# Kernel optimization log

Hardware: AMD Instinct MI355X
Metric: run time of the kernel (lower is better)

Reference implementation:

```python
import jax, jax.numpy as jnp
import numpy as np

X_DIM, H_DIM, SEQ, BATCH = 38, 128, 128, 2048


def _gru_step(h, x_t, Wih, Whh, bih, bhh):
    # PyTorch GRUCell: gates ordered (r, z, n)
    gi = x_t @ Wih.T + bih          # [B, 3H]
    gh = h @ Whh.T + bhh            # [B, 3H]
    gi_r, gi_z, gi_n = jnp.split(gi, 3, axis=-1)
    gh_r, gh_z, gh_n = jnp.split(gh, 3, axis=-1)
    r = jax.nn.sigmoid(gi_r + gh_r)
    z = jax.nn.sigmoid(gi_z + gh_z)
    n = jnp.tanh(gi_n + r * gh_n)
    return (1.0 - z) * n + z * h


def setup_inputs() -> dict:
    key = jax.random.key(0)
    ks = jax.random.split(key, 12)
    s_x = 1.0 / np.sqrt(H_DIM)
    inp = {
        "x": jax.random.normal(ks[0], (BATCH, SEQ, X_DIM), dtype=jnp.float32),
        "enc_Wih": jax.random.uniform(ks[1], (3 * H_DIM, X_DIM), minval=-s_x, maxval=s_x, dtype=jnp.float32),
        "enc_Whh": jax.random.uniform(ks[2], (3 * H_DIM, H_DIM), minval=-s_x, maxval=s_x, dtype=jnp.float32),
        "enc_bih": jax.random.uniform(ks[3], (3 * H_DIM,), minval=-s_x, maxval=s_x, dtype=jnp.float32),
        "enc_bhh": jax.random.uniform(ks[4], (3 * H_DIM,), minval=-s_x, maxval=s_x, dtype=jnp.float32),
        "dec_Wih": jax.random.uniform(ks[5], (3 * H_DIM, X_DIM), minval=-s_x, maxval=s_x, dtype=jnp.float32),
        "dec_Whh": jax.random.uniform(ks[6], (3 * H_DIM, H_DIM), minval=-s_x, maxval=s_x, dtype=jnp.float32),
        "dec_bih": jax.random.uniform(ks[7], (3 * H_DIM,), minval=-s_x, maxval=s_x, dtype=jnp.float32),
        "dec_bhh": jax.random.uniform(ks[8], (3 * H_DIM,), minval=-s_x, maxval=s_x, dtype=jnp.float32),
        "lin_W": jax.random.uniform(ks[9], (X_DIM, H_DIM), minval=-s_x, maxval=s_x, dtype=jnp.float32),
        "lin_b": jax.random.uniform(ks[10], (X_DIM,), minval=-s_x, maxval=s_x, dtype=jnp.float32),
    }
    return inp


def reference(x, enc_Wih, enc_Whh, enc_bih, enc_bhh,
              dec_Wih, dec_Whh, dec_bih, dec_bhh, lin_W, lin_b):
    B, T, _ = x.shape
    H = enc_Whh.shape[1]
    X = x.shape[-1]
    xs = jnp.swapaxes(x, 0, 1)  # [T, B, X]

    # Encoder: scan GRUCell over time, h0 = zeros
    def enc_step(h, x_t):
        h = _gru_step(h, x_t, enc_Wih, enc_Whh, enc_bih, enc_bhh)
        return h, None
    h0 = jnp.zeros((B, H), dtype=x.dtype)
    h_enc, _ = jax.lax.scan(enc_step, h0, xs)

    def dec_step(carry, _):
        h, o_prev = carry
        h = _gru_step(h, o_prev, dec_Wih, dec_Whh, dec_bih, dec_bhh)
        o = h @ lin_W.T + lin_b  # [B, X]
        return (h, o), o
    go = jnp.zeros((B, X), dtype=x.dtype)
    _, outs = jax.lax.scan(dec_step, (h_enc, go), None, length=T)  # [T, B, X]
    return jnp.swapaxes(outs, 0, 1)  # [B, T, X]
```

## Files before the change

### kernel.cpp

```cpp
#include <hip/hip_runtime.h>
#include <cstdint>


#define T_SEQ 128
#define X_DIM 38
#define H_DIM 128
#define B_TOT 2048
#define BT    8
#define HS    136
#define XK    40
#define XCH   64

#define HB_BYTES   (2 * BT * HS * 2)
#define XC_BYTES   ((XCH + 1) * BT * XK * 2)
#define SMEM_BYTES (HB_BYTES + XC_BYTES)

typedef _Float16 half8 __attribute__((ext_vector_type(8)));
typedef float    f32x4 __attribute__((ext_vector_type(4)));

#define MF(a, b, c) __builtin_amdgcn_mfma_f32_16x16x32_f16((a), (b), (c), 0, 0, 0)

__device__ __forceinline__ float fast_sigmoid(float x) {
    return __builtin_amdgcn_rcpf(1.0f + __expf(-x));
}
__device__ __forceinline__ float fast_tanh(float x) {
    return 1.0f - 2.0f * __builtin_amdgcn_rcpf(1.0f + __expf(2.0f * x));
}

#define XG_CALC(TLOC, OUTr, OUTz, OUTn)                                        \
    do {                                                                       \
        const _Float16* xr_ = xchunk + ((TLOC) * BT + arow) * XK;              \
        half8 x0_ = *(const half8*)(xr_ + quad * 8);                           \
        half8 x1_ = *(const half8*)(xr_ + 32);                                 \
        OUTr = MF(x0_, wxe[0][0], vb_r);                                       \
        OUTr = MF(x1_, wxe[0][1], OUTr);                                       \
        OUTz = MF(x0_, wxe[1][0], vb_z);                                       \
        OUTz = MF(x1_, wxe[1][1], OUTz);                                       \
        OUTn = MF(x0_, wxe[2][0], vb_ngi);                                     \
        OUTn = MF(x1_, wxe[2][1], OUTn);                                       \
    } while (0)

#define ENC_STEP(HRD, HWR, TLOC, INr, INz, INn, OUTr, OUTz, OUTn)              \
    do {                                                                       \
        const _Float16* xn_ = xchunk + (((TLOC) + 1) * BT + arow) * XK;        \
        half8 xn0_ = *(const half8*)(xn_ + quad * 8);                          \
        half8 xn1_ = *(const half8*)(xn_ + 32);                                \
        const _Float16* hb_ = (HRD) + arow * HS + quad * 8;                    \
        half8 h0_ = *(const half8*)(hb_ + 0 * 32);                             \
        half8 h1_ = *(const half8*)(hb_ + 1 * 32);                             \
        half8 h2_ = *(const half8*)(hb_ + 2 * 32);                             \
        half8 h3_ = *(const half8*)(hb_ + 3 * 32);                             \
        f32x4 ar_ = MF(h0_, wh[0][0], INr);                                    \
        ar_ = MF(h1_, wh[0][1], ar_);                                          \
        f32x4 arB_ = MF(h2_, wh[0][2], vzero);                                 \
        arB_ = MF(h3_, wh[0][3], arB_);                                        \
        f32x4 az_ = MF(h0_, wh[1][0], INz);                                    \
        az_ = MF(h1_, wh[1][1], az_);                                          \
        f32x4 azB_ = MF(h2_, wh[1][2], vzero);                                 \
        azB_ = MF(h3_, wh[1][3], azB_);                                        \
        f32x4 gn_ = MF(h0_, wh[2][0], vb_ngh);                                 \
        gn_ = MF(h1_, wh[2][1], gn_);                                          \
        f32x4 gnB_ = MF(h2_, wh[2][2], vzero);                                 \
        gnB_ = MF(h3_, wh[2][3], gnB_);                                        \
        _Pragma("unroll")                                                      \
        for (int e_ = 0; e_ < 2; ++e_) {                                       \
            const int rg_ = 2 * e_;           \
            const float r_ = fast_sigmoid(ar_[rg_] + arB_[rg_]);               \
            const float z_ = fast_sigmoid(az_[rg_] + azB_[rg_]);               \
            const float n_ = fast_tanh(INn[rg_] + r_ * (gn_[rg_] + gnB_[rg_]));\
            const float h_ = n_ + z_ * (hold[e_] - n_);                        \
            hold[e_] = h_;                                                     \
            (HWR)[(2 * quad + e_) * HS + j] = (_Float16)h_;                    \
        }                                                                      \
        OUTr = MF(xn0_, wxe[0][0], vb_r);           \
        OUTr = MF(xn1_, wxe[0][1], OUTr);           \
        OUTz = MF(xn0_, wxe[1][0], vb_z);                                      \
        OUTz = MF(xn1_, wxe[1][1], OUTz);                                      \
        OUTn = MF(xn0_, wxe[2][0], vb_ngi);                                    \
        OUTn = MF(xn1_, wxe[2][1], OUTn);                                      \
        __syncthreads();                                                       \
    } while (0)

#define DEC_STEP(HRD, HWR, TOUT)                                               \
    do {                                                                       \
        const _Float16* hb_ = (HRD) + arow * HS + quad * 8;                    \
        half8 h0_ = *(const half8*)(hb_ + 0 * 32);                             \
        half8 h1_ = *(const half8*)(hb_ + 1 * 32);                             \
        half8 h2_ = *(const half8*)(hb_ + 2 * 32);                             \
        half8 h3_ = *(const half8*)(hb_ + 3 * 32);                             \
        if (wv < 3) {             \
            f32x4 al_ = MF(h0_, wl[0], vb_lb);                                 \
            al_ = MF(h1_, wl[1], al_);                                         \
            f32x4 alB_ = MF(h2_, wl[2], vzero);                                \
            alB_ = MF(h3_, wl[3], alB_);                                       \
            if (nv) {                                                          \
                out[obase0 + (size_t)(TOUT) * X_DIM] = al_[0] + alB_[0];       \
                out[obase1 + (size_t)(TOUT) * X_DIM] = al_[2] + alB_[2];       \
            }                                                                  \
        }                                                                      \
        f32x4 ar_ = MF(h0_, wh[0][0], vd_r);                                   \
        ar_ = MF(h1_, wh[0][1], ar_);                                          \
        f32x4 arB_ = MF(h2_, wh[0][2], vzero);                                 \
        arB_ = MF(h3_, wh[0][3], arB_);                                        \
        f32x4 az_ = MF(h0_, wh[1][0], vd_z);                                   \
        az_ = MF(h1_, wh[1][1], az_);                                          \
        f32x4 azB_ = MF(h2_, wh[1][2], vzero);                                 \
        azB_ = MF(h3_, wh[1][3], azB_);                                        \
        f32x4 gn_ = MF(h0_, wh[2][0], vd_gh);                                  \
        gn_ = MF(h1_, wh[2][1], gn_);                                          \
        f32x4 gnB_ = MF(h2_, wh[2][2], vzero);                                 \
        gnB_ = MF(h3_, wh[2][3], gnB_);                                        \
        f32x4 gi_ = MF(h0_, wxn[0], vd_gi);                                    \
        gi_ = MF(h1_, wxn[1], gi_);                                            \
        f32x4 giB_ = MF(h2_, wxn[2], vzero);                                   \
        giB_ = MF(h3_, wxn[3], giB_);                                          \
        _Pragma("unroll")                                                      \
        for (int e_ = 0; e_ < 2; ++e_) {                                       \
            const int rg_ = 2 * e_;                                            \
            const float r_ = fast_sigmoid(ar_[rg_] + arB_[rg_]);               \
            const float z_ = fast_sigmoid(az_[rg_] + azB_[rg_]);               \
            const float n_ = fast_tanh((gi_[rg_] + giB_[rg_]) +                \
                                       r_ * (gn_[rg_] + gnB_[rg_]));           \
            const float h_ = n_ + z_ * (hold[e_] - n_);                        \
            hold[e_] = h_;                                                     \
            (HWR)[(2 * quad + e_) * HS + j] = (_Float16)h_;                    \
        }                                                                      \
        __syncthreads();                                                       \
    } while (0)

__global__ __launch_bounds__(512, 2)
void rae_gru_kernel(const float* __restrict__ x,
                    const float* __restrict__ eWih, const float* __restrict__ eWhh,
                    const float* __restrict__ ebih, const float* __restrict__ ebhh,
                    const float* __restrict__ dWih, const float* __restrict__ dWhh,
                    const float* __restrict__ dbih, const float* __restrict__ dbhh,
                    const float* __restrict__ linW, const float* __restrict__ linb,
                    float* __restrict__ out)
{
    __shared__ __align__(16) unsigned char smem[SMEM_BYTES];
    _Float16* const hbuf0  = (_Float16*)smem;
    _Float16* const hbuf1  = hbuf0 + BT * HS;
    _Float16* const xchunk = (_Float16*)(smem + HB_BYTES);
    _Float16* const w2lds  = xchunk;

    const int tid  = threadIdx.x;
    const int wv   = tid >> 6;
    const int ln   = tid & 63;
    const int quad = ln >> 4;
    const int mrow = ln & 15;
    const int b0   = blockIdx.x * BT;
    const int arow = mrow >> 1;
    const int j    = wv * 16 + mrow;
    const int jc0  = j, jc1 = H_DIM + j, jc2 = 2 * H_DIM + j;

    {
        uint32_t* hz = (uint32_t*)smem;
        #pragma unroll 1
        for (int i = tid; i < SMEM_BYTES / 4; i += 512) hz[i] = 0u;
    }

    auto stage_x = [&](int tb) {
        const int st = tid & 63, sr = tid >> 6;
        const float* src = x + ((size_t)(b0 + sr) * T_SEQ + tb + st) * X_DIM;
        _Float16* dst = xchunk + ((size_t)st * BT + sr) * XK;
        float v[38];
        #pragma unroll
        for (int u = 0; u < 19; ++u) {
            float2 w = *(const float2*)(src + 2 * u);
            v[2 * u] = w.x; v[2 * u + 1] = w.y;
        }
        #pragma unroll
        for (int c = 0; c < 4; ++c) {
            half8 hv;
            #pragma unroll
            for (int e = 0; e < 8; ++e) hv[e] = (_Float16)v[c * 8 + e];
            *(half8*)(dst + c * 8) = hv;
        }
        {
            half8 hv;
            #pragma unroll
            for (int e = 0; e < 6; ++e) hv[e] = (_Float16)v[32 + e];
            hv[6] = (_Float16)0.0f; hv[7] = (_Float16)0.0f;
            *(half8*)(dst + 32) = hv;
        }
    };
    stage_x(0);

    half8 wh[3][4];
    half8 wxe[3][2];
    half8 wxn[4];
    half8 wl[4];
    const f32x4 vzero = { 0.f, 0.f, 0.f, 0.f };

    #pragma unroll
    for (int p = 0; p < 3; ++p) {
        const int jp = p * H_DIM + j;
        const float* wr = eWhh + (size_t)jp * H_DIM;
        #pragma unroll
        for (int c = 0; c < 4; ++c) {
            const int kb = c * 32 + quad * 8;
            half8 v;
            #pragma unroll
            for (int e = 0; e < 8; ++e) v[e] = (_Float16)wr[kb + e];
            wh[p][c] = v;
        }
        const float* wir = eWih + (size_t)jp * X_DIM;
        #pragma unroll
        for (int c = 0; c < 2; ++c) {
            const int kb = c * 32 + quad * 8;
            half8 v;
            #pragma unroll
            for (int e = 0; e < 8; ++e) {
                const int k = kb + e;
                v[e] = (k < X_DIM) ? (_Float16)wir[k] : (_Float16)0.0f;
            }
            wxe[p][c] = v;
        }
    }
    const float eb_r   = ebih[jc0] + ebhh[jc0];
    const float eb_z   = ebih[jc1] + ebhh[jc1];
    const float eb_ngi = ebih[jc2];
    const float eb_ngh = ebhh[jc2];
    const f32x4 vb_r   = { eb_r, eb_r, eb_r, eb_r };
    const f32x4 vb_z   = { eb_z, eb_z, eb_z, eb_z };
    const f32x4 vb_ngi = { eb_ngi, eb_ngi, eb_ngi, eb_ngi };
    const f32x4 vb_ngh = { eb_ngh, eb_ngh, eb_ngh, eb_ngh };

    float hold[2] = { 0.0f, 0.0f };

    __syncthreads();

    f32x4 xgAr, xgAz, xgAn, xgBr, xgBz, xgBn;
    #pragma unroll 1
    for (int ch = 0; ch < 2; ++ch) {
        XG_CALC(0, xgAr, xgAz, xgAn);
        #pragma unroll 1
        for (int i = 0; i < 32; ++i) {
            ENC_STEP(hbuf0, hbuf1, 2 * i,     xgAr, xgAz, xgAn, xgBr, xgBz, xgBn);
            ENC_STEP(hbuf1, hbuf0, 2 * i + 1, xgBr, xgBz, xgBn, xgAr, xgAz, xgAn);
        }
        if (ch == 0) {
            stage_x(XCH);
            __syncthreads();
        }
    }

    #pragma unroll
    for (int p = 0; p < 3; ++p) {
        const float* wr = dWhh + (size_t)(p * H_DIM + j) * H_DIM;
        #pragma unroll
        for (int c = 0; c < 4; ++c) {
            const int kb = c * 32 + quad * 8;
            half8 v;
            #pragma unroll
            for (int e = 0; e < 8; ++e) v[e] = (_Float16)wr[kb + e];
            wh[p][c] = v;
        }
    }
    const float c_r0 = dbih[jc0] + dbhh[jc0];
    const float c_z0 = dbih[jc1] + dbhh[jc1];
    const float c_n0 = dbih[jc2];
    const float d_ngh = dbhh[jc2];
    const f32x4 vd_gh = { d_ngh, d_ngh, d_ngh, d_ngh };

    {
        const _Float16* hb_ = hbuf0 + arow * HS + quad * 8;
        half8 h0_ = *(const half8*)(hb_ + 0 * 32);
        half8 h1_ = *(const half8*)(hb_ + 1 * 32);
        half8 h2_ = *(const half8*)(hb_ + 2 * 32);
        half8 h3_ = *(const half8*)(hb_ + 3 * 32);
        f32x4 ar_ = { c_r0, c_r0, c_r0, c_r0 };
        ar_ = MF(h0_, wh[0][0], ar_);
        ar_ = MF(h1_, wh[0][1], ar_);
        f32x4 arB_ = MF(h2_, wh[0][2], vzero);
        arB_ = MF(h3_, wh[0][3], arB_);
        f32x4 az_ = { c_z0, c_z0, c_z0, c_z0 };
        az_ = MF(h0_, wh[1][0], az_);
        az_ = MF(h1_, wh[1][1], az_);
        f32x4 azB_ = MF(h2_, wh[1][2], vzero);
        azB_ = MF(h3_, wh[1][3], azB_);
        f32x4 gn_ = MF(h0_, wh[2][0], vd_gh);
        gn_ = MF(h1_, wh[2][1], gn_);
        f32x4 gnB_ = MF(h2_, wh[2][2], vzero);
        gnB_ = MF(h3_, wh[2][3], gnB_);
        #pragma unroll
        for (int e_ = 0; e_ < 2; ++e_) {
            const int rg_ = 2 * e_;
            const float r_ = fast_sigmoid(ar_[rg_] + arB_[rg_]);
            const float z_ = fast_sigmoid(az_[rg_] + azB_[rg_]);
            const float n_ = fast_tanh(c_n0 + r_ * (gn_[rg_] + gnB_[rg_]));
            const float h_ = n_ + z_ * (hold[e_] - n_);
            hold[e_] = h_;
            hbuf1[(2 * quad + e_) * HS + j] = (_Float16)h_;
        }
    }
    __syncthreads();

    {
        const int kk = ((wv & 1) << 6) | ln;
        const int jb = (wv >> 1) * 32;
        float lc[X_DIM];
        #pragma unroll
        for (int m = 0; m < X_DIM; ++m) lc[m] = linW[m * H_DIM + kk];

        #pragma unroll 1
        for (int jj = 0; jj < 32; ++jj) {
            const int jr = __builtin_amdgcn_readfirstlane(jb + jj);
            const float* dwr = dWih + (size_t)jr * X_DIM;
            float sacc = dWhh[(size_t)jr * H_DIM + kk];
            #pragma unroll
            for (int m = 0; m < X_DIM; ++m) sacc += dwr[m] * lc[m];
            w2lds[jr * H_DIM + kk] = (_Float16)sacc;
        }
        __syncthreads();
        #pragma unroll
        for (int c = 0; c < 4; ++c)
            wh[0][c] = *(const half8*)&w2lds[j * H_DIM + c * 32 + quad * 8];
        __syncthreads();

        #pragma unroll 1
        for (int jj = 0; jj < 32; ++jj) {
            const int jr = __builtin_amdgcn_readfirstlane(jb + jj);
            const float* dwr = dWih + (size_t)(H_DIM + jr) * X_DIM;
            float sacc = dWhh[(size_t)(H_DIM + jr) * H_DIM + kk];
            #pragma unroll
            for (int m = 0; m < X_DIM; ++m) sacc += dwr[m] * lc[m];
            w2lds[jr * H_DIM + kk] = (_Float16)sacc;
        }
        __syncthreads();
        #pragma unroll
        for (int c = 0; c < 4; ++c)
            wh[1][c] = *(const half8*)&w2lds[j * H_DIM + c * 32 + quad * 8];
        __syncthreads();

        #pragma unroll 1
        for (int jj = 0; jj < 32; ++jj) {
            const int jr = __builtin_amdgcn_readfirstlane(jb + jj);
            const float* dwr = dWih + (size_t)(2 * H_DIM + jr) * X_DIM;
            float sacc = 0.0f;
            #pragma unroll
            for (int m = 0; m < X_DIM; ++m) sacc += dwr[m] * lc[m];
            w2lds[jr * H_DIM + kk] = (_Float16)sacc;
        }
        __syncthreads();
        #pragma unroll
        for (int c = 0; c < 4; ++c)
            wxn[c] = *(const half8*)&w2lds[j * H_DIM + c * 32 + quad * 8];
        __syncthreads();
    }

    const int nlin = wv * 16 + mrow;
    const bool nv = (wv < 3) && (nlin < X_DIM);
    float lb = 0.0f;
    {
        const float* lr = linW + (size_t)(nv ? nlin : 0) * H_DIM;
        #pragma unroll
        for (int c = 0; c < 4; ++c) {
            const int kb = c * 32 + quad * 8;
            half8 v;
            #pragma unroll
            for (int e = 0; e < 8; ++e)
                v[e] = nv ? (_Float16)lr[kb + e] : (_Float16)0.0f;
            wl[c] = v;
        }
        if (nv) lb = linb[nlin];
    }
    float db_r, db_z, db_gi;
    {
        float bf[3];
        #pragma unroll
        for (int p = 0; p < 3; ++p) {
            const float* dwr = dWih + (size_t)(p * H_DIM + j) * X_DIM;
            float sacc = 0.0f;
            #pragma unroll
            for (int m = 0; m < X_DIM; ++m) sacc += linb[m] * dwr[m];
            bf[p] = sacc;
        }
        db_r  = c_r0 + bf[0];
        db_z  = c_z0 + bf[1];
        db_gi = c_n0 + bf[2];
    }
    const f32x4 vd_r  = { db_r, db_r, db_r, db_r };
    const f32x4 vd_z  = { db_z, db_z, db_z, db_z };
    const f32x4 vd_gi = { db_gi, db_gi, db_gi, db_gi };
    const f32x4 vb_lb = { lb, lb, lb, lb };

    const size_t obase0 = ((size_t)(b0 + 2 * quad)     * T_SEQ) * X_DIM + nlin;
    const size_t obase1 = ((size_t)(b0 + 2 * quad + 1) * T_SEQ) * X_DIM + nlin;

    #pragma unroll 1
    for (int i = 0; i < 63; ++i) {
        DEC_STEP(hbuf1, hbuf0, 2 * i);
        DEC_STEP(hbuf0, hbuf1, 2 * i + 1);
    }
    DEC_STEP(hbuf1, hbuf0, 126);

    if (wv < 3) {
        const _Float16* hb_ = hbuf0 + arow * HS + quad * 8;
        half8 h0_ = *(const half8*)(hb_ + 0 * 32);
        half8 h1_ = *(const half8*)(hb_ + 1 * 32);
        half8 h2_ = *(const half8*)(hb_ + 2 * 32);
        half8 h3_ = *(const half8*)(hb_ + 3 * 32);
        f32x4 al_ = MF(h0_, wl[0], vb_lb);
        al_ = MF(h1_, wl[1], al_);
        f32x4 alB_ = MF(h2_, wl[2], vzero);
        alB_ = MF(h3_, wl[3], alB_);
        if (nv) {
            out[obase0 + (size_t)(T_SEQ - 1) * X_DIM] = al_[0] + alB_[0];
            out[obase1 + (size_t)(T_SEQ - 1) * X_DIM] = al_[2] + alB_[2];
        }
    }
}

extern "C" void kernel_launch(void* const* d_in, const int* in_sizes, int n_in,
                              void* d_out, int out_size, void* d_ws, size_t ws_size,
                              hipStream_t stream) {
    (void)in_sizes; (void)n_in; (void)d_ws; (void)ws_size; (void)out_size;
    const float* x    = (const float*)d_in[0];
    const float* eWih = (const float*)d_in[1];
    const float* eWhh = (const float*)d_in[2];
    const float* ebih = (const float*)d_in[3];
    const float* ebhh = (const float*)d_in[4];
    const float* dWih = (const float*)d_in[5];
    const float* dWhh = (const float*)d_in[6];
    const float* dbih = (const float*)d_in[7];
    const float* dbhh = (const float*)d_in[8];
    const float* linW = (const float*)d_in[9];
    const float* linb = (const float*)d_in[10];
    float* out = (float*)d_out;

    rae_gru_kernel<<<dim3(B_TOT / BT), dim3(512), 0, stream>>>(
        x, eWih, eWhh, ebih, ebhh, dWih, dWhh, dbih, dbhh, linW, linb, out);
}
```

Baseline: 291.3 us.

## Pre-scale gate weights by log2e, defer output stores, and transpose x staging

Gate weights and biases are pre-multiplied by log2(e) (or 2·log2(e) for the candidate gate) so the activations can use exp2f directly, dropping one multiply per activation. The decoder's output projection is moved after the gate math and its global store is deferred to the next step, which takes the store off the recurrent critical path. The x staging thread mapping is transposed so consecutive threads handle consecutive batch rows. Scaling the weights before the fp16 cast changes rounding slightly.

After: 303.9 us. +4.3%, slower.

```diff
diff --git a/kernel.cpp b/kernel.cpp
--- a/kernel.cpp
+++ b/kernel.cpp
@@ -11,6 +11,9 @@
 #define XK    40
 #define XCH   64
 
+#define S1 1.44269504088896f
+#define S2 2.88539008177793f
+
 #define HB_BYTES   (2 * BT * HS * 2)
 #define XC_BYTES   ((XCH + 1) * BT * XK * 2)
 #define SMEM_BYTES (HB_BYTES + XC_BYTES)
@@ -20,11 +23,11 @@
 
 #define MF(a, b, c) __builtin_amdgcn_mfma_f32_16x16x32_f16((a), (b), (c), 0, 0, 0)
 
-__device__ __forceinline__ float fast_sigmoid(float x) {
-    return __builtin_amdgcn_rcpf(1.0f + __expf(-x));
+__device__ __forceinline__ float sig2(float s) {
+    return __builtin_amdgcn_rcpf(1.0f + exp2f(-s));
 }
-__device__ __forceinline__ float fast_tanh(float x) {
-    return 1.0f - 2.0f * __builtin_amdgcn_rcpf(1.0f + __expf(2.0f * x));
+__device__ __forceinline__ float tanh2(float s) {
+    return 1.0f - 2.0f * __builtin_amdgcn_rcpf(1.0f + exp2f(s));
 }
 
 #define XG_CALC(TLOC, OUTr, OUTz, OUTn)                                        \
@@ -65,9 +68,9 @@
         _Pragma("unroll")                                                      \
         for (int e_ = 0; e_ < 2; ++e_) {                                       \
             const int rg_ = 2 * e_;           \
-            const float r_ = fast_sigmoid(ar_[rg_] + arB_[rg_]);               \
-            const float z_ = fast_sigmoid(az_[rg_] + azB_[rg_]);               \
-            const float n_ = fast_tanh(INn[rg_] + r_ * (gn_[rg_] + gnB_[rg_]));\
+            const float r_ = sig2(ar_[rg_] + arB_[rg_]);                       \
+            const float z_ = sig2(az_[rg_] + azB_[rg_]);                       \
+            const float n_ = tanh2(INn[rg_] + r_ * (gn_[rg_] + gnB_[rg_]));    \
             const float h_ = n_ + z_ * (hold[e_] - n_);                        \
             hold[e_] = h_;                                                     \
             (HWR)[(2 * quad + e_) * HS + j] = (_Float16)h_;                    \
@@ -81,23 +84,17 @@
         __syncthreads();                                                       \
     } while (0)
 
-#define DEC_STEP(HRD, HWR, TOUT)                                               \
+#define DEC_STEP(HRD, HWR, TPREV, SP)                                          \
     do {                                                                       \
+        if ((SP) && nv) {                                                      \
+            out[obase0 + (size_t)(TPREV) * X_DIM] = po0;                       \
+            out[obase1 + (size_t)(TPREV) * X_DIM] = po1;                       \
+        }                                                                      \
         const _Float16* hb_ = (HRD) + arow * HS + quad * 8;                    \
         half8 h0_ = *(const half8*)(hb_ + 0 * 32);                             \
         half8 h1_ = *(const half8*)(hb_ + 1 * 32);                             \
         half8 h2_ = *(const half8*)(hb_ + 2 * 32);                             \
         half8 h3_ = *(const half8*)(hb_ + 3 * 32);                             \
-        if (wv < 3) {             \
-            f32x4 al_ = MF(h0_, wl[0], vb_lb);                                 \
-            al_ = MF(h1_, wl[1], al_);                                         \
-            f32x4 alB_ = MF(h2_, wl[2], vzero);                                \
-            alB_ = MF(h3_, wl[3], alB_);                                       \
-            if (nv) {                                                          \
-                out[obase0 + (size_t)(TOUT) * X_DIM] = al_[0] + alB_[0];       \
-                out[obase1 + (size_t)(TOUT) * X_DIM] = al_[2] + alB_[2];       \
-            }                                                                  \
-        }                                                                      \
         f32x4 ar_ = MF(h0_, wh[0][0], vd_r);                                   \
         ar_ = MF(h1_, wh[0][1], ar_);                                          \
         f32x4 arB_ = MF(h2_, wh[0][2], vzero);                                 \
@@ -117,13 +114,21 @@
         _Pragma("unroll")                                                      \
         for (int e_ = 0; e_ < 2; ++e_) {                                       \
             const int rg_ = 2 * e_;                                            \
-            const float r_ = fast_sigmoid(ar_[rg_] + arB_[rg_]);               \
-            const float z_ = fast_sigmoid(az_[rg_] + azB_[rg_]);               \
-            const float n_ = fast_tanh((gi_[rg_] + giB_[rg_]) +                \
-                                       r_ * (gn_[rg_] + gnB_[rg_]));           \
+            const float r_ = sig2(ar_[rg_] + arB_[rg_]);                       \
+            const float z_ = sig2(az_[rg_] + azB_[rg_]);                       \
+            const float n_ = tanh2((gi_[rg_] + giB_[rg_]) +                    \
+                                   r_ * (gn_[rg_] + gnB_[rg_]));               \
             const float h_ = n_ + z_ * (hold[e_] - n_);                        \
             hold[e_] = h_;                                                     \
             (HWR)[(2 * quad + e_) * HS + j] = (_Float16)h_;                    \
+        }                                                                      \
+        if (wv < 3) {    \
+            f32x4 al_ = MF(h0_, wl[0], vb_lb);                                 \
+            al_ = MF(h1_, wl[1], al_);                                         \
+            f32x4 alB_ = MF(h2_, wl[2], vzero);                                \
+            alB_ = MF(h3_, wl[3], alB_);                                       \
+            po0 = al_[0] + alB_[0];                                            \
+            po1 = al_[2] + alB_[2];                                            \
         }                                                                      \
         __syncthreads();                                                       \
     } while (0)
@@ -160,7 +165,7 @@
     }
 
     auto stage_x = [&](int tb) {
-        const int st = tid & 63, sr = tid >> 6;
+        const int sr = tid & 7, st = tid >> 3;
         const float* src = x + ((size_t)(b0 + sr) * T_SEQ + tb + st) * X_DIM;
         _Float16* dst = xchunk + ((size_t)st * BT + sr) * XK;
         float v[38];
@@ -194,6 +199,7 @@
 
     #pragma unroll
     for (int p = 0; p < 3; ++p) {
+        const float sc = (p == 2) ? S2 : S1;
         const int jp = p * H_DIM + j;
         const float* wr = eWhh + (size_t)jp * H_DIM;
         #pragma unroll
@@ -201,7 +207,7 @@
             const int kb = c * 32 + quad * 8;
             half8 v;
             #pragma unroll
-            for (int e = 0; e < 8; ++e) v[e] = (_Float16)wr[kb + e];
+            for (int e = 0; e < 8; ++e) v[e] = (_Float16)(sc * wr[kb + e]);
             wh[p][c] = v;
         }
         const float* wir = eWih + (size_t)jp * X_DIM;
@@ -212,15 +218,15 @@
             #pragma unroll
             for (int e = 0; e < 8; ++e) {
                 const int k = kb + e;
-                v[e] = (k < X_DIM) ? (_Float16)wir[k] : (_Float16)0.0f;
+                v[e] = (k < X_DIM) ? (_Float16)(sc * wir[k]) : (_Float16)0.0f;
             }
             wxe[p][c] = v;
         }
     }
-    const float eb_r   = ebih[jc0] + ebhh[jc0];
-    const float eb_z   = ebih[jc1] + ebhh[jc1];
-    const float eb_ngi = ebih[jc2];
-    const float eb_ngh = ebhh[jc2];
+    const float eb_r   = S1 * (ebih[jc0] + ebhh[jc0]);
+    const float eb_z   = S1 * (ebih[jc1] + ebhh[jc1]);
+    const float eb_ngi = S2 * ebih[jc2];
+    const float eb_ngh = S2 * ebhh[jc2];
     const f32x4 vb_r   = { eb_r, eb_r, eb_r, eb_r };
     const f32x4 vb_z   = { eb_z, eb_z, eb_z, eb_z };
     const f32x4 vb_ngi = { eb_ngi, eb_ngi, eb_ngi, eb_ngi };
@@ -247,20 +253,21 @@
 
     #pragma unroll
     for (int p = 0; p < 3; ++p) {
+        const float sc = (p == 2) ? S2 : S1;
         const float* wr = dWhh + (size_t)(p * H_DIM + j) * H_DIM;
         #pragma unroll
         for (int c = 0; c < 4; ++c) {
             const int kb = c * 32 + quad * 8;
             half8 v;
             #pragma unroll
-            for (int e = 0; e < 8; ++e) v[e] = (_Float16)wr[kb + e];
+            for (int e = 0; e < 8; ++e) v[e] = (_Float16)(sc * wr[kb + e]);
             wh[p][c] = v;
         }
     }
-    const float c_r0 = dbih[jc0] + dbhh[jc0];
-    const float c_z0 = dbih[jc1] + dbhh[jc1];
-    const float c_n0 = dbih[jc2];
-    const float d_ngh = dbhh[jc2];
+    const float c_r0 = S1 * (dbih[jc0] + dbhh[jc0]);
+    const float c_z0 = S1 * (dbih[jc1] + dbhh[jc1]);
+    const float c_n0 = S2 * dbih[jc2];
+    const float d_ngh = S2 * dbhh[jc2];
     const f32x4 vd_gh = { d_ngh, d_ngh, d_ngh, d_ngh };
 
     {
@@ -286,9 +293,9 @@
         #pragma unroll
         for (int e_ = 0; e_ < 2; ++e_) {
             const int rg_ = 2 * e_;
-            const float r_ = fast_sigmoid(ar_[rg_] + arB_[rg_]);
-            const float z_ = fast_sigmoid(az_[rg_] + azB_[rg_]);
-            const float n_ = fast_tanh(c_n0 + r_ * (gn_[rg_] + gnB_[rg_]));
+            const float r_ = sig2(ar_[rg_] + arB_[rg_]);
+            const float z_ = sig2(az_[rg_] + azB_[rg_]);
+            const float n_ = tanh2(c_n0 + r_ * (gn_[rg_] + gnB_[rg_]));
             const float h_ = n_ + z_ * (hold[e_] - n_);
             hold[e_] = h_;
             hbuf1[(2 * quad + e_) * HS + j] = (_Float16)h_;
@@ -310,7 +317,7 @@
             float sacc = dWhh[(size_t)jr * H_DIM + kk];
             #pragma unroll
             for (int m = 0; m < X_DIM; ++m) sacc += dwr[m] * lc[m];
-            w2lds[jr * H_DIM + kk] = (_Float16)sacc;
+            w2lds[jr * H_DIM + kk] = (_Float16)(S1 * sacc);
         }
         __syncthreads();
         #pragma unroll
@@ -325,7 +332,7 @@
             float sacc = dWhh[(size_t)(H_DIM + jr) * H_DIM + kk];
             #pragma unroll
             for (int m = 0; m < X_DIM; ++m) sacc += dwr[m] * lc[m];
-            w2lds[jr * H_DIM + kk] = (_Float16)sacc;
+            w2lds[jr * H_DIM + kk] = (_Float16)(S1 * sacc);
         }
         __syncthreads();
         #pragma unroll
@@ -340,7 +347,7 @@
             float sacc = 0.0f;
             #pragma unroll
             for (int m = 0; m < X_DIM; ++m) sacc += dwr[m] * lc[m];
-            w2lds[jr * H_DIM + kk] = (_Float16)sacc;
+            w2lds[jr * H_DIM + kk] = (_Float16)(S2 * sacc);
         }
         __syncthreads();
         #pragma unroll
@@ -376,9 +383,9 @@
             for (int m = 0; m < X_DIM; ++m) sacc += linb[m] * dwr[m];
             bf[p] = sacc;
         }
-        db_r  = c_r0 + bf[0];
-        db_z  = c_z0 + bf[1];
-        db_gi = c_n0 + bf[2];
+        db_r  = c_r0 + S1 * bf[0];
+        db_z  = c_z0 + S1 * bf[1];
+        db_gi = c_n0 + S2 * bf[2];
     }
     const f32x4 vd_r  = { db_r, db_r, db_r, db_r };
     const f32x4 vd_z  = { db_z, db_z, db_z, db_z };
@@ -388,13 +395,18 @@
     const size_t obase0 = ((size_t)(b0 + 2 * quad)     * T_SEQ) * X_DIM + nlin;
     const size_t obase1 = ((size_t)(b0 + 2 * quad + 1) * T_SEQ) * X_DIM + nlin;
 
+    float po0 = 0.0f, po1 = 0.0f;
+    DEC_STEP(hbuf1, hbuf0, 0, 0);
     #pragma unroll 1
     for (int i = 0; i < 63; ++i) {
-        DEC_STEP(hbuf1, hbuf0, 2 * i);
-        DEC_STEP(hbuf0, hbuf1, 2 * i + 1);
-    }
-    DEC_STEP(hbuf1, hbuf0, 126);
-
+        DEC_STEP(hbuf0, hbuf1, 2 * i,     1);
+        DEC_STEP(hbuf1, hbuf0, 2 * i + 1, 1);
+    }
+
+    if (nv) {
+        out[obase0 + (size_t)126 * X_DIM] = po0;
+        out[obase1 + (size_t)126 * X_DIM] = po1;
+    }
     if (wv < 3) {
         const _Float16* hb_ = hbuf0 + arow * HS + quad * 8;
         half8 h0_ = *(const half8*)(hb_ + 0 * 32);
```
